# Optimization experiments

Hardware: AMD Instinct MI355X
Metric: run time of the kernel (lower is better)

Reference implementation:

```python
import jax, jax.numpy as jnp
import numpy as np

N_NODES = 10000
N_EDGES = 320000
DIM = 256
NUM_HEADS = 8
HEAD_DIM = DIM // NUM_HEADS


def setup_inputs() -> dict:
    key = jax.random.key(0)
    ks = jax.random.split(key, 8)
    s = 1.0 / np.sqrt(DIM)
    x = jax.random.normal(ks[0], (N_NODES, DIM), dtype=jnp.float32)
    src = jax.random.randint(ks[1], (N_EDGES,), 0, N_NODES, dtype=jnp.int32)
    dst = jax.random.randint(ks[2], (N_EDGES,), 0, N_NODES, dtype=jnp.int32)
    Wq = jax.random.normal(ks[3], (DIM, DIM), dtype=jnp.float32) * s
    Wk = jax.random.normal(ks[4], (DIM, DIM), dtype=jnp.float32) * s
    Wv = jax.random.normal(ks[5], (DIM, DIM), dtype=jnp.float32) * s
    Wo = jax.random.normal(ks[6], (DIM, DIM), dtype=jnp.float32) * s
    z = jnp.zeros((DIM,), dtype=jnp.float32)
    return {"x": x, "src": src, "dst": dst,
            "Wq": Wq, "bq": z, "Wk": Wk, "bk": z,
            "Wv": Wv, "bv": z, "Wo": Wo, "bo": z}


def reference(x, src, dst, Wq, bq, Wk, bk, Wv, bv, Wo, bo):
    N = x.shape[0]
    # nn.Linear: y = x @ W.T + b
    q = (x @ Wq.T + bq).reshape(N, NUM_HEADS, HEAD_DIM)
    k = (x @ Wk.T + bk).reshape(N, NUM_HEADS, HEAD_DIM)
    v = (x @ Wv.T + bv).reshape(N, NUM_HEADS, HEAD_DIM)
    # u_dot_v: dot(q[src], k[dst]) per head -> [E, H]
    score = jnp.einsum('ehd,ehd->eh', q[src], k[dst]) / np.sqrt(HEAD_DIM).astype(np.float32)
    # Faithful to source: F.softmax(dim=1) on [E, H, 1] -> softmax over HEADS axis
    attn = jax.nn.softmax(score, axis=1)  # [E, H]
    # u_mul_e then sum-reduce onto destination nodes
    m = v[src] * attn[:, :, None]  # [E, H, HEAD_DIM]
    h = jax.ops.segment_sum(m, dst, num_segments=N).reshape(N, DIM)
    out = h @ Wo.T + bo
    # dropout p=0.0 -> identity
    return out
```

## Files before the change

### kernel.cpp

```cpp
#include <hip/hip_runtime.h>
#include <stdint.h>

#define N_NODES 10000
#define N_EDGES 320000
#define DIM 256
#define NRANGE 4
#define RANGE_DIV 2500
#define PAD_SLOTS 32

typedef _Float16 half8 __attribute__((ext_vector_type(8)));
typedef _Float16 half2t __attribute__((ext_vector_type(2)));
typedef float floatx4 __attribute__((ext_vector_type(4)));

#define QK_SCALE 0.17677669529663687f

typedef __attribute__((address_space(3))) uint32_t lds_u32;
typedef __attribute__((address_space(1))) const uint32_t glob_u32;
__device__ __forceinline__ void load16_lds(const _Float16* g, _Float16* l) {
  __builtin_amdgcn_global_load_lds((glob_u32*)g, (lds_u32*)l, 16, 0, 0);
}

__device__ __forceinline__ half8 cvt8s(const float4 a, const float4 b, float sc) {
  half8 o;
  o[0] = (_Float16)(a.x * sc); o[1] = (_Float16)(a.y * sc);
  o[2] = (_Float16)(a.z * sc); o[3] = (_Float16)(a.w * sc);
  o[4] = (_Float16)(b.x * sc); o[5] = (_Float16)(b.y * sc);
  o[6] = (_Float16)(b.z * sc); o[7] = (_Float16)(b.w * sc);
  return o;
}

__global__ void __launch_bounds__(256) prep_k(
    const float* __restrict__ x, const float* __restrict__ Wq,
    const float* __restrict__ Wk, const float* __restrict__ Wv,
    const float* __restrict__ Wo, const int* __restrict__ src,
    const int* __restrict__ dst,
    _Float16* __restrict__ xh, _Float16* __restrict__ Wcat,
    _Float16* __restrict__ Woh, int* __restrict__ cnt4,
    int* __restrict__ slist4) {
  int b = blockIdx.x;
  int t = threadIdx.x;
  if (b < 1250) {
    int i = b * 256 + t;
    const float4* p = (const float4*)x;
    ((half8*)xh)[i] = cvt8s(p[2 * i], p[2 * i + 1], 1.0f);
  } else if (b < 1378) {
    int bb = b - 1250;
    int w = bb >> 5;
    int i = (bb & 31) * 256 + t;
    const float* in = (w == 0) ? Wq : (w == 1) ? Wv : (w == 2) ? Wk : Wo;
    _Float16* out = (w < 3) ? (Wcat + (size_t)w * 65536) : Woh;
    float sc = (w == 0) ? QK_SCALE : 1.0f;
    const float4* p = (const float4*)in;
    ((half8*)out)[i] = cvt8s(p[2 * i], p[2 * i + 1], sc);
  } else {
    int e = (b - 1378) * 256 + t;
    int s = src[e];
    int r = s / RANGE_DIV;
    int cell = dst[e] * NRANGE + r;
    int pos = atomicAdd(&cnt4[cell], 1);
    if (pos < PAD_SLOTS) slist4[cell * PAD_SLOTS + pos] = s;
  }
}

template <int MODE>
__global__ void __launch_bounds__(256) gemm_tiled(
    const _Float16* __restrict__ A, const _Float16* __restrict__ B,
    const float* __restrict__ b0, const float* __restrict__ b1,
    const float* __restrict__ b2,
    _Float16* __restrict__ qv, _Float16* __restrict__ kh,
    float* __restrict__ outf, int M) {
  __shared__ _Float16 As[16384];
  __shared__ _Float16 Bs[16384];
  int t = threadIdx.x;
  int lane = t & 63;
  int wid = t >> 6;
  int l16 = lane & 15;
  int quad = lane >> 4;
  int wm = wid >> 1, wn = wid & 1;
  int m0 = blockIdx.x * 128;
  int n0 = blockIdx.y * 128;

  floatx4 acc[4][4];
#pragma unroll
  for (int i = 0; i < 4; ++i)
#pragma unroll
    for (int j = 0; j < 4; ++j) acc[i][j] = (floatx4){0.f, 0.f, 0.f, 0.f};

  auto stage = [&](int ks, int buf) {
#pragma unroll
    for (int i = 0; i < 4; ++i) {
      int idx = i * 4 + wid;
      int c = idx >> 1;
      int h = idx & 1;
      int r = h * 64 + lane;
      int ar = m0 + r;
      if (ar >= M) ar = M - 1;
      load16_lds(A + (size_t)ar * 256 + ks * 64 + c * 8,
                 &As[buf * 8192 + (c * 128 + h * 64) * 8]);
      load16_lds(B + (size_t)(n0 + r) * 256 + ks * 64 + c * 8,
                 &Bs[buf * 8192 + (c * 128 + h * 64) * 8]);
    }
  };

  stage(0, 0);
  __syncthreads();

  for (int ks = 0; ks < 4; ++ks) {
    int bsel = ks & 1;
    if (ks < 3) stage(ks + 1, 1 - bsel);
#pragma unroll
    for (int kk = 0; kk < 2; ++kk) {
      int j = kk * 4 + quad;
      half8 af[4], bf[4];
#pragma unroll
      for (int i = 0; i < 4; ++i) {
        af[i] = *(const half8*)&As[bsel * 8192 + (j * 128 + wm * 64 + i * 16 + l16) * 8];
        bf[i] = *(const half8*)&Bs[bsel * 8192 + (j * 128 + wn * 64 + i * 16 + l16) * 8];
      }
#pragma unroll
      for (int mi = 0; mi < 4; ++mi)
#pragma unroll
        for (int ni = 0; ni < 4; ++ni)
          acc[mi][ni] =
              __builtin_amdgcn_mfma_f32_16x16x32_f16(af[mi], bf[ni], acc[mi][ni], 0, 0, 0);
    }
    __syncthreads();
  }

#pragma unroll
  for (int mi = 0; mi < 4; ++mi) {
#pragma unroll
    for (int ni = 0; ni < 4; ++ni) {
      int col = n0 + wn * 64 + ni * 16 + l16;
      float bias;
      if (MODE == 0) {
        bias = (col < 256) ? b0[col] * QK_SCALE
                           : (col < 512) ? b1[col - 256] : b2[col - 512];
      } else {
        bias = b0[col];
      }
#pragma unroll
      for (int r = 0; r < 4; ++r) {
        int row = m0 + wm * 64 + mi * 16 + quad * 4 + r;
        if (row < M) {
          float val = acc[mi][ni][r] + bias;
          if (MODE == 0) {
            if (col < 512)
              qv[(size_t)row * 512 + col] = (_Float16)val;
            else
              kh[(size_t)row * 256 + (col - 512)] = (_Float16)val;
          } else {
            outf[(size_t)row * 256 + col] = val;
          }
        }
      }
    }
  }
}

__global__ void __launch_bounds__(256, 4) aggregate_k(
    const _Float16* __restrict__ qv, const _Float16* __restrict__ kh,
    const int* __restrict__ slist4, const int* __restrict__ cnt4,
    _Float16* __restrict__ hh) {
  int lane = threadIdx.x & 63;
  int n = blockIdx.x * 4 + (threadIdx.x >> 6);
  if (n >= N_NODES) return;
  int h = lane & 7;
  int g = lane >> 3;

  int4 cv = ((const int4*)cnt4)[n];
  int d0 = min(cv.x, PAD_SLOTS), d1 = min(cv.y, PAD_SLOTS);
  int d2 = min(cv.z, PAD_SLOTS), d3 = min(cv.w, PAD_SLOTS);
  int o1 = d0, o2 = o1 + d1, o3 = o2 + d2;
  int T = o3 + d3;
  const int* nb = slist4 + (size_t)n * (NRANGE * PAD_SLOTS);

  int sidA = 0, sidB = 0;
  {
    int i0 = lane;
    int r0 = (i0 >= o1) + (i0 >= o2) + (i0 >= o3);
    int b0r = (r0 == 0) ? 0 : (r0 == 1) ? o1 : (r0 == 2) ? o2 : o3;
    if (i0 < T) sidA = nb[r0 * PAD_SLOTS + (i0 - b0r)];
    if (T > 64) {
      int i1 = lane + 64;
      int r1 = (i1 >= o1) + (i1 >= o2) + (i1 >= o3);
      int b1r = (r1 == 0) ? 0 : (r1 == 1) ? o1 : (r1 == 2) ? o2 : o3;
      if (i1 < T) sidB = nb[r1 * PAD_SLOTS + (i1 - b1r)];
    }
  }

  half8 kc[4];
  const half8* krow = (const half8*)(kh + (size_t)n * DIM + h * 32);
#pragma unroll
  for (int i = 0; i < 4; ++i) kc[i] = krow[i];
  const half2t* k2 = (const half2t*)kc;

  half2t acc[16];
#pragma unroll
  for (int i = 0; i < 16; ++i) acc[i] = (half2t){(_Float16)0.f, (_Float16)0.f};

  int iters = (T + 7) >> 3;
  if (iters > 0) {
    int s = __shfl(sidA, g);
    const half8* rr = (const half8*)(qv + (size_t)s * 512 + h * 32);
    half8 qc[4], vc[4];
#pragma unroll
    for (int i = 0; i < 4; ++i) { qc[i] = rr[i]; vc[i] = rr[32 + i]; }
    bool valid = g < T;

#pragma unroll 1
    for (int jj = 0; jj < iters; ++jj) {
      half8 nq[4], nv[4];
      bool nvalid = false;
      if (jj + 1 < iters) {
        int nidx = (jj + 1) * 8 + g;
        int ns = (jj + 1 < 8) ? __shfl(sidA, nidx) : __shfl(sidB, nidx - 64);
        const half8* nr = (const half8*)(qv + (size_t)ns * 512 + h * 32);
#pragma unroll
        for (int i = 0; i < 4; ++i) { nq[i] = nr[i]; nv[i] = nr[32 + i]; }
        nvalid = nidx < T;
      }
      const half2t* q2 = (const half2t*)qc;
      float pa = 0.f, pb = 0.f, pc = 0.f, pd = 0.f;
#pragma unroll
      for (int i = 0; i < 4; ++i) {
#if __has_builtin(__builtin_amdgcn_fdot2)
        pa = __builtin_amdgcn_fdot2(q2[i], k2[i], pa, false);
        pb = __builtin_amdgcn_fdot2(q2[4 + i], k2[4 + i], pb, false);
        pc = __builtin_amdgcn_fdot2(q2[8 + i], k2[8 + i], pc, false);
        pd = __builtin_amdgcn_fdot2(q2[12 + i], k2[12 + i], pd, false);
#else
        pa += (float)q2[i][0] * (float)k2[i][0] + (float)q2[i][1] * (float)k2[i][1];
        pb += (float)q2[4 + i][0] * (float)k2[4 + i][0] + (float)q2[4 + i][1] * (float)k2[4 + i][1];
        pc += (float)q2[8 + i][0] * (float)k2[8 + i][0] + (float)q2[8 + i][1] * (float)k2[8 + i][1];
        pd += (float)q2[12 + i][0] * (float)k2[12 + i][0] + (float)q2[12 + i][1] * (float)k2[12 + i][1];
#endif
      }
      float p = (pa + pb) + (pc + pd);
      float ex = __expf(p);
      float ssum = ex;
      ssum += __shfl_xor(ssum, 1);
      ssum += __shfl_xor(ssum, 2);
      ssum += __shfl_xor(ssum, 4);
      float a = valid ? (ex * __frcp_rn(ssum)) : 0.f;
      _Float16 ah = (_Float16)a;
      half2t ah2 = (half2t){ah, ah};
      const half2t* v2 = (const half2t*)vc;
#pragma unroll
      for (int i = 0; i < 16; ++i) acc[i] += v2[i] * ah2;
#pragma unroll
      for (int i = 0; i < 4; ++i) { qc[i] = nq[i]; vc[i] = nv[i]; }
      valid = nvalid;
    }
  }

#pragma unroll
  for (int i = 0; i < 16; ++i) {
    union { half2t h2; int v; } u;
    u.h2 = acc[i]; u.v = __shfl_xor(u.v, 8);  acc[i] += u.h2;
    u.h2 = acc[i]; u.v = __shfl_xor(u.v, 16); acc[i] += u.h2;
    u.h2 = acc[i]; u.v = __shfl_xor(u.v, 32); acc[i] += u.h2;
  }
  if (g == 0) {
    half8* hrow = (half8*)(hh + (size_t)n * DIM + h * 32);
    const half8* a8 = (const half8*)acc;
#pragma unroll
    for (int i = 0; i < 4; ++i) hrow[i] = a8[i];
  }
}

extern "C" void kernel_launch(void* const* d_in, const int* in_sizes, int n_in,
                              void* d_out, int out_size, void* d_ws, size_t ws_size,
                              hipStream_t stream) {
  const float* x = (const float*)d_in[0];
  const int* src = (const int*)d_in[1];
  const int* dst = (const int*)d_in[2];
  const float* Wq = (const float*)d_in[3];
  const float* bq = (const float*)d_in[4];
  const float* Wk = (const float*)d_in[5];
  const float* bk = (const float*)d_in[6];
  const float* Wv = (const float*)d_in[7];
  const float* bv = (const float*)d_in[8];
  const float* Wo = (const float*)d_in[9];
  const float* bo = (const float*)d_in[10];

  char* p = (char*)d_ws;
  const size_t SZ_NODE_H = (size_t)N_NODES * DIM * sizeof(_Float16);
  _Float16* xh = (_Float16*)p; p += SZ_NODE_H;
  _Float16* qvv = (_Float16*)p; p += 2 * SZ_NODE_H;
  _Float16* kh = (_Float16*)p; p += SZ_NODE_H;
  _Float16* hh = (_Float16*)p; p += SZ_NODE_H;
  _Float16* Wcat = (_Float16*)p; p += (size_t)768 * 256 * sizeof(_Float16);
  _Float16* Woh = (_Float16*)p; p += (size_t)256 * 256 * sizeof(_Float16);
  int* cnt4 = (int*)p; p += (size_t)N_NODES * NRANGE * sizeof(int);
  int* slist4 = (int*)p; p += (size_t)N_NODES * NRANGE * PAD_SLOTS * sizeof(int);

  hipMemsetAsync(cnt4, 0, (size_t)N_NODES * NRANGE * sizeof(int), stream);

  prep_k<<<2628, 256, 0, stream>>>(x, Wq, Wk, Wv, Wo, src, dst, xh, Wcat, Woh,
                                   cnt4, slist4);

  gemm_tiled<0><<<dim3(79, 6), 256, 0, stream>>>(xh, Wcat, bq, bv, bk, qvv, kh,
                                                 nullptr, N_NODES);

  aggregate_k<<<2500, 256, 0, stream>>>(qvv, kh, slist4, cnt4, hh);

  gemm_tiled<1><<<dim3(79, 2), 256, 0, stream>>>(hh, Woh, bo, nullptr, nullptr,
                                                 nullptr, nullptr, (float*)d_out,
                                                 N_NODES);
}
```

Before: 172.5 us.

## Fuse all stages into one persistent cooperative kernel with grid syncs

```diff
diff --git a/kernel.cpp b/kernel.cpp
--- a/kernel.cpp
+++ b/kernel.cpp
@@ -1,5 +1,8 @@
 #include <hip/hip_runtime.h>
+#include <hip/hip_cooperative_groups.h>
 #include <stdint.h>
+
+namespace cg = cooperative_groups;
 
 #define N_NODES 10000
 #define N_EDGES 320000
@@ -29,93 +32,63 @@
   return o;
 }
 
-__global__ void __launch_bounds__(256) prep_k(
-    const float* __restrict__ x, const float* __restrict__ Wq,
-    const float* __restrict__ Wk, const float* __restrict__ Wv,
-    const float* __restrict__ Wo, const int* __restrict__ src,
-    const int* __restrict__ dst,
-    _Float16* __restrict__ xh, _Float16* __restrict__ Wcat,
-    _Float16* __restrict__ Woh, int* __restrict__ cnt4,
-    int* __restrict__ slist4) {
-  int b = blockIdx.x;
-  int t = threadIdx.x;
-  if (b < 1250) {
-    int i = b * 256 + t;
-    const float4* p = (const float4*)x;
-    ((half8*)xh)[i] = cvt8s(p[2 * i], p[2 * i + 1], 1.0f);
-  } else if (b < 1378) {
-    int bb = b - 1250;
-    int w = bb >> 5;
-    int i = (bb & 31) * 256 + t;
-    const float* in = (w == 0) ? Wq : (w == 1) ? Wv : (w == 2) ? Wk : Wo;
-    _Float16* out = (w < 3) ? (Wcat + (size_t)w * 65536) : Woh;
-    float sc = (w == 0) ? QK_SCALE : 1.0f;
-    const float4* p = (const float4*)in;
-    ((half8*)out)[i] = cvt8s(p[2 * i], p[2 * i + 1], sc);
-  } else {
-    int e = (b - 1378) * 256 + t;
-    int s = src[e];
-    int r = s / RANGE_DIV;
-    int cell = dst[e] * NRANGE + r;
-    int pos = atomicAdd(&cnt4[cell], 1);
-    if (pos < PAD_SLOTS) slist4[cell * PAD_SLOTS + pos] = s;
-  }
-}
-
-template <int MODE>
-__global__ void __launch_bounds__(256) gemm_tiled(
-    const _Float16* __restrict__ A, const _Float16* __restrict__ B,
-    const float* __restrict__ b0, const float* __restrict__ b1,
-    const float* __restrict__ b2,
-    _Float16* __restrict__ qv, _Float16* __restrict__ kh,
-    float* __restrict__ outf, int M) {
-  __shared__ _Float16 As[16384];
-  __shared__ _Float16 Bs[16384];
-  int t = threadIdx.x;
-  int lane = t & 63;
-  int wid = t >> 6;
-  int l16 = lane & 15;
-  int quad = lane >> 4;
-  int wm = wid >> 1, wn = wid & 1;
-  int m0 = blockIdx.x * 128;
-  int n0 = blockIdx.y * 128;
-
-  floatx4 acc[4][4];
-#pragma unroll
-  for (int i = 0; i < 4; ++i)
-#pragma unroll
-    for (int j = 0; j < 4; ++j) acc[i][j] = (floatx4){0.f, 0.f, 0.f, 0.f};
-
-  auto stage = [&](int ks, int buf) {
-#pragma unroll
-    for (int i = 0; i < 4; ++i) {
-      int idx = i * 4 + wid;
-      int c = idx >> 1;
-      int h = idx & 1;
-      int r = h * 64 + lane;
-      int ar = m0 + r;
-      if (ar >= M) ar = M - 1;
-      load16_lds(A + (size_t)ar * 256 + ks * 64 + c * 8,
-                 &As[buf * 8192 + (c * 128 + h * 64) * 8]);
-      load16_lds(B + (size_t)(n0 + r) * 256 + ks * 64 + c * 8,
-                 &Bs[buf * 8192 + (c * 128 + h * 64) * 8]);
-    }
-  };
-
-  stage(0, 0);
-  __syncthreads();
-
-  for (int ks = 0; ks < 4; ++ks) {
-    int bsel = ks & 1;
-    if (ks < 3) stage(ks + 1, 1 - bsel);
-#pragma unroll
-    for (int kk = 0; kk < 2; ++kk) {
-      int j = kk * 4 + quad;
+struct Params {
+  const float *x, *Wq, *Wk, *Wv, *Wo;
+  const float *bq, *bk, *bv, *bo;
+  const int *src, *dst;
+  _Float16 *xh, *Wcat, *Woh, *qv, *kh, *hh;
+  int *cnt4, *slist4;
+  float* outf;
+};
+
+__global__ void __launch_bounds__(256, 4) fused_k(Params P) {
+  cg::grid_group grid = cg::this_grid();
+  __shared__ _Float16 As[8192];
+  __shared__ _Float16 Bs[8192];
+
+  const int t = threadIdx.x;
+  const int bid = blockIdx.x;
+  const int G = gridDim.x;
+  const int lane = t & 63, wid = t >> 6;
+  const int l16 = lane & 15, quad = lane >> 4;
+  const int wm = wid >> 1, wn = wid & 1;
+
+  auto gemm_tile = [&](int mode, int bx, int by, const _Float16* A, const _Float16* B,
+                       const float* c0, const float* c1, const float* c2) {
+    int m0 = bx * 128, n0 = by * 128;
+    floatx4 acc[4][4];
+#pragma unroll
+    for (int i = 0; i < 4; ++i)
+#pragma unroll
+      for (int j = 0; j < 4; ++j) acc[i][j] = (floatx4){0.f, 0.f, 0.f, 0.f};
+
+    auto stage = [&](int ks, int buf) {
+#pragma unroll
+      for (int i = 0; i < 2; ++i) {
+        int idx = i * 4 + wid;
+        int c = idx >> 1;
+        int hh2 = idx & 1;
+        int r = hh2 * 64 + lane;
+        int ar = m0 + r;
+        if (ar >= N_NODES) ar = N_NODES - 1;
+        load16_lds(A + (size_t)ar * 256 + ks * 32 + c * 8,
+                   &As[buf * 4096 + (c * 128 + hh2 * 64) * 8]);
+        load16_lds(B + (size_t)(n0 + r) * 256 + ks * 32 + c * 8,
+                   &Bs[buf * 4096 + (c * 128 + hh2 * 64) * 8]);
+      }
+    };
+
+    stage(0, 0);
+    __syncthreads();
+
+    for (int ks = 0; ks < 8; ++ks) {
+      int bsel = ks & 1;
+      if (ks < 7) stage(ks + 1, 1 - bsel);
       half8 af[4], bf[4];
 #pragma unroll
       for (int i = 0; i < 4; ++i) {
-        af[i] = *(const half8*)&As[bsel * 8192 + (j * 128 + wm * 64 + i * 16 + l16) * 8];
-        bf[i] = *(const half8*)&Bs[bsel * 8192 + (j * 128 + wn * 64 + i * 16 + l16) * 8];
+        af[i] = *(const half8*)&As[bsel * 4096 + (quad * 128 + wm * 64 + i * 16 + l16) * 8];
+        bf[i] = *(const half8*)&Bs[bsel * 4096 + (quad * 128 + wn * 64 + i * 16 + l16) * 8];
       }
 #pragma unroll
       for (int mi = 0; mi < 4; ++mi)
@@ -123,167 +96,209 @@
         for (int ni = 0; ni < 4; ++ni)
           acc[mi][ni] =
               __builtin_amdgcn_mfma_f32_16x16x32_f16(af[mi], bf[ni], acc[mi][ni], 0, 0, 0);
-    }
-    __syncthreads();
+      __syncthreads();
+    }
+
+#pragma unroll
+    for (int mi = 0; mi < 4; ++mi) {
+#pragma unroll
+      for (int ni = 0; ni < 4; ++ni) {
+        int col = n0 + wn * 64 + ni * 16 + l16;
+        float bias;
+        if (mode == 0) {
+          bias = (col < 256) ? c0[col] * QK_SCALE
+                             : (col < 512) ? c1[col - 256] : c2[col - 512];
+        } else {
+          bias = c0[col];
+        }
+#pragma unroll
+        for (int r = 0; r < 4; ++r) {
+          int row = m0 + wm * 64 + mi * 16 + quad * 4 + r;
+          if (row < N_NODES) {
+            float val = acc[mi][ni][r] + bias;
+            if (mode == 0) {
+              if (col < 512)
+                P.qv[(size_t)row * 512 + col] = (_Float16)val;
+              else
+                P.kh[(size_t)row * 256 + (col - 512)] = (_Float16)val;
+            } else {
+              P.outf[(size_t)row * 256 + col] = val;
+            }
+          }
+        }
+      }
+    }
+  };
+
+  {
+    int gt = bid * 256 + t;
+    int gs = G * 256;
+    const int V = 320000 + 32768 + 10000;
+    for (int i = gt; i < V; i += gs) {
+      if (i < 320000) {
+        const float4* p = (const float4*)P.x;
+        ((half8*)P.xh)[i] = cvt8s(p[2 * i], p[2 * i + 1], 1.0f);
+      } else if (i < 352768) {
+        int u = i - 320000;
+        int w = u >> 13;
+        int j = u & 8191;
+        const float* in = (w == 0) ? P.Wq : (w == 1) ? P.Wv : (w == 2) ? P.Wk : P.Wo;
+        _Float16* out = (w < 3) ? (P.Wcat + (size_t)w * 65536) : P.Woh;
+        float sc = (w == 0) ? QK_SCALE : 1.0f;
+        const float4* p = (const float4*)in;
+        ((half8*)out)[j] = cvt8s(p[2 * j], p[2 * j + 1], sc);
+      } else {
+        ((int4*)P.cnt4)[i - 352768] = (int4){0, 0, 0, 0};
+      }
+    }
   }
-
-#pragma unroll
-  for (int mi = 0; mi < 4; ++mi) {
-#pragma unroll
-    for (int ni = 0; ni < 4; ++ni) {
-      int col = n0 + wn * 64 + ni * 16 + l16;
-      float bias;
-      if (MODE == 0) {
-        bias = (col < 256) ? b0[col] * QK_SCALE
-                           : (col < 512) ? b1[col - 256] : b2[col - 512];
+  __threadfence();
+  grid.sync();
+
+  {
+    const int CE = 582;
+    for (int u = bid; u < 1024; u += G) {
+      if (u < 474) {
+        gemm_tile(0, u % 79, u / 79, P.xh, P.Wcat, P.bq, P.bv, P.bk);
       } else {
-        bias = b0[col];
-      }
-#pragma unroll
-      for (int r = 0; r < 4; ++r) {
-        int row = m0 + wm * 64 + mi * 16 + quad * 4 + r;
-        if (row < M) {
-          float val = acc[mi][ni][r] + bias;
-          if (MODE == 0) {
-            if (col < 512)
-              qv[(size_t)row * 512 + col] = (_Float16)val;
-            else
-              kh[(size_t)row * 256 + (col - 512)] = (_Float16)val;
-          } else {
-            outf[(size_t)row * 256 + col] = val;
+        int e0 = (u - 474) * CE;
+        int e1 = e0 + CE;
+        if (e1 > N_EDGES) e1 = N_EDGES;
+        for (int e = e0 + t; e < e1; e += 256) {
+          int s = P.src[e];
+          int r = s / RANGE_DIV;
+          int cell = P.dst[e] * NRANGE + r;
+          int pos = atomicAdd(&P.cnt4[cell], 1);
+          if (pos < PAD_SLOTS) P.slist4[cell * PAD_SLOTS + pos] = s;
+        }
+      }
+    }
+  }
+  __threadfence();
+  grid.sync();
+
+  {
+    const int h = lane & 7;
+    const int g = lane >> 3;
+    for (int nb = bid; nb < 2500; nb += G) {
+      int n = nb * 4 + wid;
+
+      int4 cv = ((const int4*)P.cnt4)[n];
+      int d0 = min(cv.x, PAD_SLOTS), d1 = min(cv.y, PAD_SLOTS);
+      int d2 = min(cv.z, PAD_SLOTS), d3 = min(cv.w, PAD_SLOTS);
+      int o1 = d0, o2 = o1 + d1, o3 = o2 + d2;
+      int T = o3 + d3;
+      const int* nbp = P.slist4 + (size_t)n * (NRANGE * PAD_SLOTS);
+
+      int sidA = 0, sidB = 0;
+      {
+        int i0 = lane;
+        int r0 = (i0 >= o1) + (i0 >= o2) + (i0 >= o3);
+        int b0r = (r0 == 0) ? 0 : (r0 == 1) ? o1 : (r0 == 2) ? o2 : o3;
+        if (i0 < T) sidA = nbp[r0 * PAD_SLOTS + (i0 - b0r)];
+        if (T > 64) {
+          int i1 = lane + 64;
+          int r1 = (i1 >= o1) + (i1 >= o2) + (i1 >= o3);
+          int b1r = (r1 == 0) ? 0 : (r1 == 1) ? o1 : (r1 == 2) ? o2 : o3;
+          if (i1 < T) sidB = nbp[r1 * PAD_SLOTS + (i1 - b1r)];
+        }
+      }
+
+      half8 kc[4];
+      const half8* krow = (const half8*)(P.kh + (size_t)n * DIM + h * 32);
+#pragma unroll
+      for (int i = 0; i < 4; ++i) kc[i] = krow[i];
+      const half2t* k2 = (const half2t*)kc;
+
+      half2t acc[16];
+#pragma unroll
+      for (int i = 0; i < 16; ++i) acc[i] = (half2t){(_Float16)0.f, (_Float16)0.f};
+
+      int iters = (T + 7) >> 3;
+      if (iters > 0) {
+        int s0 = __shfl(sidA, g);
+        const half8* rr = (const half8*)(P.qv + (size_t)s0 * 512 + h * 32);
+        half8 qc[4];
+#pragma unroll
+        for (int i = 0; i < 4; ++i) qc[i] = rr[i];
+        bool valid = g < T;
+
+#pragma unroll 1
+        for (int jj = 0; jj < iters; ++jj) {
+          half8 vc[4];
+#pragma unroll
+          for (int i = 0; i < 4; ++i) vc[i] = rr[32 + i];
+          half8 nq[4];
+          bool nvalid = false;
+          const half8* nrr = rr;
+          if (jj + 1 < iters) {
+            int nidx = (jj + 1) * 8 + g;
+            int ns = (jj + 1 < 8) ? __shfl(sidA, nidx) : __shfl(sidB, nidx - 64);
+            nrr = (const half8*)(P.qv + (size_t)ns * 512 + h * 32);
+#pragma unroll
+            for (int i = 0; i < 4; ++i) nq[i] = nrr[i];
+            nvalid = nidx < T;
           }
-        }
+          const half2t* q2 = (const half2t*)qc;
+          float pa = 0.f, pb = 0.f, pc = 0.f, pd = 0.f;
+#pragma unroll
+          for (int i = 0; i < 4; ++i) {
+#if __has_builtin(__builtin_amdgcn_fdot2)
+            pa = __builtin_amdgcn_fdot2(q2[i], k2[i], pa, false);
+            pb = __builtin_amdgcn_fdot2(q2[4 + i], k2[4 + i], pb, false);
+            pc = __builtin_amdgcn_fdot2(q2[8 + i], k2[8 + i], pc, false);
+            pd = __builtin_amdgcn_fdot2(q2[12 + i], k2[12 + i], pd, false);
+#else
+            pa += (float)q2[i][0] * (float)k2[i][0] + (float)q2[i][1] * (float)k2[i][1];
+            pb += (float)q2[4 + i][0] * (float)k2[4 + i][0] + (float)q2[4 + i][1] * (float)k2[4 + i][1];
+            pc += (float)q2[8 + i][0] * (float)k2[8 + i][0] + (float)q2[8 + i][1] * (float)k2[8 + i][1];
+            pd += (float)q2[12 + i][0] * (float)k2[12 + i][0] + (float)q2[12 + i][1] * (float)k2[12 + i][1];
+#endif
+          }
+          float p = (pa + pb) + (pc + pd);
+          float ex = __expf(p);
+          float ssum = ex;
+          ssum += __shfl_xor(ssum, 1);
+          ssum += __shfl_xor(ssum, 2);
+          ssum += __shfl_xor(ssum, 4);
+          float a = valid ? (ex * __frcp_rn(ssum)) : 0.f;
+          _Float16 ah = (_Float16)a;
+          half2t ah2 = (half2t){ah, ah};
+          const half2t* v2 = (const half2t*)vc;
+#pragma unroll
+          for (int i = 0; i < 16; ++i) acc[i] += v2[i] * ah2;
+#pragma unroll
+          for (int i = 0; i < 4; ++i) qc[i] = nq[i];
+          rr = nrr;
+          valid = nvalid;
+        }
+      }
+
+#pragma unroll
+      for (int i = 0; i < 16; ++i) {
+        union { half2t h2; int v; } u;
+        u.h2 = acc[i]; u.v = __shfl_xor(u.v, 8);  acc[i] += u.h2;
+        u.h2 = acc[i]; u.v = __shfl_xor(u.v, 16); acc[i] += u.h2;
+        u.h2 = acc[i]; u.v = __shfl_xor(u.v, 32); acc[i] += u.h2;
+      }
+      if (g == 0) {
+        half8* hrow = (half8*)(P.hh + (size_t)n * DIM + h * 32);
+        const half8* a8 = (const half8*)acc;
+#pragma unroll
+        for (int i = 0; i < 4; ++i) hrow[i] = a8[i];
       }
     }
   }
-}
-
-__global__ void __launch_bounds__(256, 4) aggregate_k(
-    const _Float16* __restrict__ qv, const _Float16* __restrict__ kh,
-    const int* __restrict__ slist4, const int* __restrict__ cnt4,
-    _Float16* __restrict__ hh) {
-  int lane = threadIdx.x & 63;
-  int n = blockIdx.x * 4 + (threadIdx.x >> 6);
-  if (n >= N_NODES) return;
-  int h = lane & 7;
-  int g = lane >> 3;
-
-  int4 cv = ((const int4*)cnt4)[n];
-  int d0 = min(cv.x, PAD_SLOTS), d1 = min(cv.y, PAD_SLOTS);
-  int d2 = min(cv.z, PAD_SLOTS), d3 = min(cv.w, PAD_SLOTS);
-  int o1 = d0, o2 = o1 + d1, o3 = o2 + d2;
-  int T = o3 + d3;
-  const int* nb = slist4 + (size_t)n * (NRANGE * PAD_SLOTS);
-
-  int sidA = 0, sidB = 0;
-  {
-    int i0 = lane;
-    int r0 = (i0 >= o1) + (i0 >= o2) + (i0 >= o3);
-    int b0r = (r0 == 0) ? 0 : (r0 == 1) ? o1 : (r0 == 2) ? o2 : o3;
-    if (i0 < T) sidA = nb[r0 * PAD_SLOTS + (i0 - b0r)];
-    if (T > 64) {
-      int i1 = lane + 64;
-      int r1 = (i1 >= o1) + (i1 >= o2) + (i1 >= o3);
-      int b1r = (r1 == 0) ? 0 : (r1 == 1) ? o1 : (r1 == 2) ? o2 : o3;
-      if (i1 < T) sidB = nb[r1 * PAD_SLOTS + (i1 - b1r)];
-    }
-  }
-
-  half8 kc[4];
-  const half8* krow = (const half8*)(kh + (size_t)n * DIM + h * 32);
-#pragma unroll
-  for (int i = 0; i < 4; ++i) kc[i] = krow[i];
-  const half2t* k2 = (const half2t*)kc;
-
-  half2t acc[16];
-#pragma unroll
-  for (int i = 0; i < 16; ++i) acc[i] = (half2t){(_Float16)0.f, (_Float16)0.f};
-
-  int iters = (T + 7) >> 3;
-  if (iters > 0) {
-    int s = __shfl(sidA, g);
-    const half8* rr = (const half8*)(qv + (size_t)s * 512 + h * 32);
-    half8 qc[4], vc[4];
-#pragma unroll
-    for (int i = 0; i < 4; ++i) { qc[i] = rr[i]; vc[i] = rr[32 + i]; }
-    bool valid = g < T;
-
-#pragma unroll 1
-    for (int jj = 0; jj < iters; ++jj) {
-      half8 nq[4], nv[4];
-      bool nvalid = false;
-      if (jj + 1 < iters) {
-        int nidx = (jj + 1) * 8 + g;
-        int ns = (jj + 1 < 8) ? __shfl(sidA, nidx) : __shfl(sidB, nidx - 64);
-        const half8* nr = (const half8*)(qv + (size_t)ns * 512 + h * 32);
-#pragma unroll
-        for (int i = 0; i < 4; ++i) { nq[i] = nr[i]; nv[i] = nr[32 + i]; }
-        nvalid = nidx < T;
-      }
-      const half2t* q2 = (const half2t*)qc;
-      float pa = 0.f, pb = 0.f, pc = 0.f, pd = 0.f;
-#pragma unroll
-      for (int i = 0; i < 4; ++i) {
-#if __has_builtin(__builtin_amdgcn_fdot2)
-        pa = __builtin_amdgcn_fdot2(q2[i], k2[i], pa, false);
-        pb = __builtin_amdgcn_fdot2(q2[4 + i], k2[4 + i], pb, false);
-        pc = __builtin_amdgcn_fdot2(q2[8 + i], k2[8 + i], pc, false);
-        pd = __builtin_amdgcn_fdot2(q2[12 + i], k2[12 + i], pd, false);
-#else
-        pa += (float)q2[i][0] * (float)k2[i][0] + (float)q2[i][1] * (float)k2[i][1];
-        pb += (float)q2[4 + i][0] * (float)k2[4 + i][0] + (float)q2[4 + i][1] * (float)k2[4 + i][1];
-        pc += (float)q2[8 + i][0] * (float)k2[8 + i][0] + (float)q2[8 + i][1] * (float)k2[8 + i][1];
-        pd += (float)q2[12 + i][0] * (float)k2[12 + i][0] + (float)q2[12 + i][1] * (float)k2[12 + i][1];
-#endif
-      }
-      float p = (pa + pb) + (pc + pd);
-      float ex = __expf(p);
-      float ssum = ex;
-      ssum += __shfl_xor(ssum, 1);
-      ssum += __shfl_xor(ssum, 2);
-      ssum += __shfl_xor(ssum, 4);
-      float a = valid ? (ex * __frcp_rn(ssum)) : 0.f;
-      _Float16 ah = (_Float16)a;
-      half2t ah2 = (half2t){ah, ah};
-      const half2t* v2 = (const half2t*)vc;
-#pragma unroll
-      for (int i = 0; i < 16; ++i) acc[i] += v2[i] * ah2;
-#pragma unroll
-      for (int i = 0; i < 4; ++i) { qc[i] = nq[i]; vc[i] = nv[i]; }
-      valid = nvalid;
-    }
-  }
-
-#pragma unroll
-  for (int i = 0; i < 16; ++i) {
-    union { half2t h2; int v; } u;
-    u.h2 = acc[i]; u.v = __shfl_xor(u.v, 8);  acc[i] += u.h2;
-    u.h2 = acc[i]; u.v = __shfl_xor(u.v, 16); acc[i] += u.h2;
-    u.h2 = acc[i]; u.v = __shfl_xor(u.v, 32); acc[i] += u.h2;
-  }
-  if (g == 0) {
-    half8* hrow = (half8*)(hh + (size_t)n * DIM + h * 32);
-    const half8* a8 = (const half8*)acc;
-#pragma unroll
-    for (int i = 0; i < 4; ++i) hrow[i] = a8[i];
-  }
+  __threadfence();
+  grid.sync();
+
+  for (int u = bid; u < 158; u += G)
+    gemm_tile(1, u % 79, u / 79, P.hh, P.Woh, P.bo, nullptr, nullptr);
 }
 
 extern "C" void kernel_launch(void* const* d_in, const int* in_sizes, int n_in,
                               void* d_out, int out_size, void* d_ws, size_t ws_size,
                               hipStream_t stream) {
-  const float* x = (const float*)d_in[0];
-  const int* src = (const int*)d_in[1];
-  const int* dst = (const int*)d_in[2];
-  const float* Wq = (const float*)d_in[3];
-  const float* bq = (const float*)d_in[4];
-  const float* Wk = (const float*)d_in[5];
-  const float* bk = (const float*)d_in[6];
-  const float* Wv = (const float*)d_in[7];
-  const float* bv = (const float*)d_in[8];
-  const float* Wo = (const float*)d_in[9];
-  const float* bo = (const float*)d_in[10];
-
   char* p = (char*)d_ws;
   const size_t SZ_NODE_H = (size_t)N_NODES * DIM * sizeof(_Float16);
   _Float16* xh = (_Float16*)p; p += SZ_NODE_H;
@@ -295,17 +310,39 @@
   int* cnt4 = (int*)p; p += (size_t)N_NODES * NRANGE * sizeof(int);
   int* slist4 = (int*)p; p += (size_t)N_NODES * NRANGE * PAD_SLOTS * sizeof(int);
 
-  hipMemsetAsync(cnt4, 0, (size_t)N_NODES * NRANGE * sizeof(int), stream);
-
-  prep_k<<<2628, 256, 0, stream>>>(x, Wq, Wk, Wv, Wo, src, dst, xh, Wcat, Woh,
-                                   cnt4, slist4);
-
-  gemm_tiled<0><<<dim3(79, 6), 256, 0, stream>>>(xh, Wcat, bq, bv, bk, qvv, kh,
-                                                 nullptr, N_NODES);
-
-  aggregate_k<<<2500, 256, 0, stream>>>(qvv, kh, slist4, cnt4, hh);
-
-  gemm_tiled<1><<<dim3(79, 2), 256, 0, stream>>>(hh, Woh, bo, nullptr, nullptr,
-                                                 nullptr, nullptr, (float*)d_out,
-                                                 N_NODES);
+  Params prm;
+  prm.x = (const float*)d_in[0];
+  prm.src = (const int*)d_in[1];
+  prm.dst = (const int*)d_in[2];
+  prm.Wq = (const float*)d_in[3];
+  prm.bq = (const float*)d_in[4];
+  prm.Wk = (const float*)d_in[5];
+  prm.bk = (const float*)d_in[6];
+  prm.Wv = (const float*)d_in[7];
+  prm.bv = (const float*)d_in[8];
+  prm.Wo = (const float*)d_in[9];
+  prm.bo = (const float*)d_in[10];
+  prm.xh = xh; prm.Wcat = Wcat; prm.Woh = Woh;
+  prm.qv = qvv; prm.kh = kh; prm.hh = hh;
+  prm.cnt4 = cnt4; prm.slist4 = slist4;
+  prm.outf = (float*)d_out;
+
+  static int s_grid = 0;
+  if (s_grid == 0) {
+    int nb = 0;
+    if (hipOccupancyMaxActiveBlocksPerMultiprocessor(&nb, (const void*)fused_k, 256, 0) !=
+            hipSuccess || nb < 1)
+      nb = 2;
+    int dev = 0;
+    (void)hipGetDevice(&dev);
+    int ncu = 0;
+    if (hipDeviceGetAttribute(&ncu, hipDeviceAttributeMultiprocessorCount, dev) !=
+            hipSuccess || ncu < 1)
+      ncu = 256;
+    s_grid = nb * ncu;
+    if (s_grid > 2500) s_grid = 2500;
+  }
+
+  void* kp[] = {(void*)&prm};
+  hipLaunchCooperativeKernel((const void*)fused_k, dim3(s_grid), dim3(256), kp, 0, stream);
 }
```

Measured after the change: 534.7 us. 3.1x slower.
